# Performance work log

Hardware: AMD Instinct MI355X
Metric: run time of the kernel (lower is better)

The kernel has to match this reference:

```python
import jax, jax.numpy as jnp
import numpy as np

D_MODEL = 1024
MAX_ELEMENTS = 128


def setup_inputs() -> dict:
    key = jax.random.key(0)
    ks = jax.random.split(key, 12)
    B, S = 256, 128
    d, dq = D_MODEL, D_MODEL // 4
    inp = {
        "element_types": jax.random.randint(ks[0], (B, S), 0, 5, dtype=jnp.int64 if jax.config.jax_enable_x64 else jnp.int32),
        "element_indices": jax.random.randint(ks[1], (B, S), 0, MAX_ELEMENTS, dtype=jnp.int64 if jax.config.jax_enable_x64 else jnp.int32),
        "style_vectors": jax.random.normal(ks[2], (B, 5), dtype=jnp.float32),
        "page_captions": jax.random.normal(ks[3], (B, 768), dtype=jnp.float32),
        # learned parameters (torch Linear stored as [in, out] so y = x @ W + b)
        "type_emb": jax.random.normal(ks[4], (5, d), dtype=jnp.float32) * 0.02,
        "pos_emb": jax.random.normal(ks[5], (MAX_ELEMENTS, d), dtype=jnp.float32) * 0.02,
        "style_w1": jax.random.normal(ks[6], (5, dq), dtype=jnp.float32) * 0.02,
        "style_b1": jnp.zeros((dq,), dtype=jnp.float32),
        "style_w2": jax.random.normal(ks[7], (dq, d), dtype=jnp.float32) * 0.02,
        "style_b2": jnp.zeros((d,), dtype=jnp.float32),
        "text_w": jax.random.normal(ks[8], (768, d), dtype=jnp.float32) * 0.02,
        "text_b": jnp.zeros((d,), dtype=jnp.float32),
        "final_pos_emb": jax.random.normal(ks[9], (MAX_ELEMENTS, d), dtype=jnp.float32) * 0.02,
    }
    return inp


def reference(element_types, element_indices, style_vectors, page_captions,
              type_emb, pos_emb, style_w1, style_b1, style_w2, style_b2,
              text_w, text_b, final_pos_emb):
    B, S = element_types.shape
    # table gathers: [B, S, d]
    emb = type_emb[element_types] + pos_emb[element_indices]
    # per-batch style/text embeds computed ONCE (the torch loop recomputes them per step)
    style_embed = jnp.maximum(style_vectors @ style_w1 + style_b1, 0.0) @ style_w2 + style_b2  # [B, d]
    page_embed = page_captions @ text_w + text_b  # [B, d]
    # loop over i with mask (types[:, i] == 1) == broadcast masked add
    mask1 = (element_types == 1)[:, :, None]  # [B, S, 1]
    emb = emb + mask1 * (style_embed + page_embed)[:, None, :]
    # final positional encoding over positions 0..S-1
    emb = emb + final_pos_emb[:S][None, :, :]
    padding_mask = element_types == 0
    return emb, padding_mask
```

## Files before the change

kernel.cpp:

```cpp
#include <hip/hip_runtime.h>

#define D      1024
#define SEQ    128
#define BATCH  256
#define DQ     256
#define TEXTC  768

typedef float f32x4 __attribute__((ext_vector_type(4)));

__global__ __launch_bounds__(256) void gemm_fused(
    const float* __restrict__ style_vectors,
    const float* __restrict__ page_captions,
    const float* __restrict__ style_w1,
    const float* __restrict__ style_b1,
    const float* __restrict__ style_w2,
    const float* __restrict__ style_b2,
    const float* __restrict__ text_w,
    const float* __restrict__ text_b,
    float* __restrict__ part)
{
    __shared__ float As[16][68];
    __shared__ float Bs[16][68];

    const int m0  = blockIdx.x * 64;
    const int n0  = blockIdx.y * 64;
    const int z   = blockIdx.z;
    const int tid = threadIdx.x;
    const int tm  = tid >> 4;
    const int tn  = tid & 15;

    const int am = tid >> 2;
    const int ak = (tid & 3) * 4;

    float sv[5];
    if (z == 0) {
#pragma unroll
        for (int j = 0; j < 5; ++j) sv[j] = style_vectors[(m0 + am) * 5 + j];
    }

    float acc[4][4] = {};

    for (int kc = 0; kc < 256; kc += 16) {
        if (z == 0) {
            int k = kc + ak;
#pragma unroll
            for (int r = 0; r < 4; ++r) {
                float h = style_b1[k + r];
#pragma unroll
                for (int j = 0; j < 5; ++j)
                    h = fmaf(sv[j], style_w1[j * DQ + k + r], h);
                As[ak + r][am] = fmaxf(h, 0.0f);
            }
        } else {
            float4 av = *(const float4*)
                &page_captions[(m0 + am) * TEXTC + (z * 256 - DQ) + kc + ak];
            As[ak + 0][am] = av.x;
            As[ak + 1][am] = av.y;
            As[ak + 2][am] = av.z;
            As[ak + 3][am] = av.w;
        }
        {
            int kk   = tid >> 4;
            int nq   = (tid & 15) * 4;
            int krow = z * 256 + kc + kk;
            const float* Wrow = (z == 0) ? &style_w2[krow * D]
                                         : &text_w[(krow - DQ) * D];
            *(float4*)&Bs[kk][nq] = *(const float4*)&Wrow[n0 + nq];
        }
        __syncthreads();

#pragma unroll
        for (int kk = 0; kk < 16; ++kk) {
            f32x4 a4 = *(const f32x4*)&As[kk][tm * 4];
            f32x4 b4 = *(const f32x4*)&Bs[kk][tn * 4];
#pragma unroll
            for (int ii = 0; ii < 4; ++ii)
#pragma unroll
                for (int jj = 0; jj < 4; ++jj)
                    acc[ii][jj] = fmaf(a4[ii], b4[jj], acc[ii][jj]);
        }
        __syncthreads();
    }

    float* dst = part + (size_t)z * BATCH * D;
    const int n = n0 + tn * 4;
#pragma unroll
    for (int ii = 0; ii < 4; ++ii) {
        int m = m0 + tm * 4 + ii;
        f32x4 v = {acc[ii][0], acc[ii][1], acc[ii][2], acc[ii][3]};
        if (z == 0) {
            v[0] += style_b2[n + 0] + text_b[n + 0];
            v[1] += style_b2[n + 1] + text_b[n + 1];
            v[2] += style_b2[n + 2] + text_b[n + 2];
            v[3] += style_b2[n + 3] + text_b[n + 3];
        }
        *(f32x4*)&dst[m * D + n] = v;
    }
}

__global__ __launch_bounds__(256) void reduce_part(
    const float* __restrict__ part,
    float* __restrict__ comb)
{
    const int i = blockIdx.x * 256 + threadIdx.x;
    const f32x4* p = (const f32x4*)part;
    const int Q = BATCH * D / 4;
    f32x4 v = p[i] + p[i + Q] + p[i + 2 * Q] + p[i + 3 * Q];
    ((f32x4*)comb)[i] = v;
}

__global__ __launch_bounds__(256) void scatter_kernel(
    const int* __restrict__ types,
    const int* __restrict__ indices,
    const float* __restrict__ type_emb,
    const float* __restrict__ pos_emb,
    const float* __restrict__ final_pos_emb,
    const float* __restrict__ comb,
    float* __restrict__ out_emb,
    float* __restrict__ out_mask)
{
    const int bs = blockIdx.x;
    const int b  = bs >> 7;
    const int s  = bs & 127;
    const int et = types[bs];
    const int ei = indices[bs];
    const int tid = threadIdx.x;

    f32x4 t = ((const f32x4*)&type_emb[et * D])[tid];
    f32x4 p = ((const f32x4*)&pos_emb[ei * D])[tid];
    f32x4 f = ((const f32x4*)&final_pos_emb[s * D])[tid];
    f32x4 v = t + p + f;
    if (et == 1)
        v = v + ((const f32x4*)&comb[b * D])[tid];

    __builtin_nontemporal_store(v, &((f32x4*)out_emb)[bs * 256 + tid]);

    if (tid == 0)
        out_mask[bs] = (et == 0) ? 1.0f : 0.0f;
}

extern "C" void kernel_launch(void* const* d_in, const int* in_sizes, int n_in,
                              void* d_out, int out_size, void* d_ws, size_t ws_size,
                              hipStream_t stream) {
    const int*   element_types   = (const int*)  d_in[0];
    const int*   element_indices = (const int*)  d_in[1];
    const float* style_vectors   = (const float*)d_in[2];
    const float* page_captions   = (const float*)d_in[3];
    const float* type_emb        = (const float*)d_in[4];
    const float* pos_emb         = (const float*)d_in[5];
    const float* style_w1        = (const float*)d_in[6];
    const float* style_b1        = (const float*)d_in[7];
    const float* style_w2        = (const float*)d_in[8];
    const float* style_b2        = (const float*)d_in[9];
    const float* text_w          = (const float*)d_in[10];
    const float* text_b          = (const float*)d_in[11];
    const float* final_pos_emb   = (const float*)d_in[12];

    float* part = (float*)d_ws;
    float* comb = (float*)d_ws + 4 * BATCH * D;

    float* out_emb  = (float*)d_out;
    float* out_mask = (float*)d_out + BATCH * SEQ * D;

    gemm_fused<<<dim3(BATCH / 64, D / 64, 4), 256, 0, stream>>>(
        style_vectors, page_captions, style_w1, style_b1,
        style_w2, style_b2, text_w, text_b, part);

    reduce_part<<<BATCH * D / 4 / 256, 256, 0, stream>>>(part, comb);

    scatter_kernel<<<BATCH * SEQ, 256, 0, stream>>>(
        element_types, element_indices, type_emb, pos_emb, final_pos_emb,
        comb, out_emb, out_mask);
}
```

Measured before the change: 206.9 us.

## Halve GEMM M-tile, use nontemporal reduce loads, one wave per row in scatter

The GEMM tile shrinks from 64 to 32 rows, doubling the block count to 512 so more CUs have work; only half the threads now load the A tile. The reduce kernel reads its partials with nontemporal loads. The scatter kernel now assigns one wave per (b,s) row, four rows per block, so the grid is four times smaller and each lane handles four vectors. The style branch is hoisted so it is uniform per wave.

New measurement: 199.9 us, median of 2. 3.4% less time.

```diff
diff --git a/kernel.cpp b/kernel.cpp
--- a/kernel.cpp
+++ b/kernel.cpp
@@ -7,6 +7,7 @@
 #define TEXTC  768
 
 typedef float f32x4 __attribute__((ext_vector_type(4)));
+typedef float f32x2 __attribute__((ext_vector_type(2)));
 
 __global__ __launch_bounds__(256) void gemm_fused(
     const float* __restrict__ style_vectors,
@@ -19,10 +20,10 @@
     const float* __restrict__ text_b,
     float* __restrict__ part)
 {
-    __shared__ float As[16][68];
+    __shared__ float As[16][36];
     __shared__ float Bs[16][68];
 
-    const int m0  = blockIdx.x * 64;
+    const int m0  = blockIdx.x * 32;
     const int n0  = blockIdx.y * 64;
     const int z   = blockIdx.z;
     const int tid = threadIdx.x;
@@ -33,31 +34,33 @@
     const int ak = (tid & 3) * 4;
 
     float sv[5];
-    if (z == 0) {
+    if (z == 0 && tid < 128) {
 #pragma unroll
         for (int j = 0; j < 5; ++j) sv[j] = style_vectors[(m0 + am) * 5 + j];
     }
 
-    float acc[4][4] = {};
+    float acc[2][4] = {};
 
     for (int kc = 0; kc < 256; kc += 16) {
-        if (z == 0) {
-            int k = kc + ak;
+        if (tid < 128) {
+            if (z == 0) {
+                int k = kc + ak;
 #pragma unroll
-            for (int r = 0; r < 4; ++r) {
-                float h = style_b1[k + r];
+                for (int r = 0; r < 4; ++r) {
+                    float h = style_b1[k + r];
 #pragma unroll
-                for (int j = 0; j < 5; ++j)
-                    h = fmaf(sv[j], style_w1[j * DQ + k + r], h);
-                As[ak + r][am] = fmaxf(h, 0.0f);
+                    for (int j = 0; j < 5; ++j)
+                        h = fmaf(sv[j], style_w1[j * DQ + k + r], h);
+                    As[ak + r][am] = fmaxf(h, 0.0f);
+                }
+            } else {
+                float4 av = *(const float4*)
+                    &page_captions[(m0 + am) * TEXTC + (z * 256 - DQ) + kc + ak];
+                As[ak + 0][am] = av.x;
+                As[ak + 1][am] = av.y;
+                As[ak + 2][am] = av.z;
+                As[ak + 3][am] = av.w;
             }
-        } else {
-            float4 av = *(const float4*)
-                &page_captions[(m0 + am) * TEXTC + (z * 256 - DQ) + kc + ak];
-            As[ak + 0][am] = av.x;
-            As[ak + 1][am] = av.y;
-            As[ak + 2][am] = av.z;
-            As[ak + 3][am] = av.w;
         }
         {
             int kk   = tid >> 4;
@@ -71,13 +74,13 @@
 
 #pragma unroll
         for (int kk = 0; kk < 16; ++kk) {
-            f32x4 a4 = *(const f32x4*)&As[kk][tm * 4];
+            f32x2 a2 = *(const f32x2*)&As[kk][tm * 2];
             f32x4 b4 = *(const f32x4*)&Bs[kk][tn * 4];
 #pragma unroll
-            for (int ii = 0; ii < 4; ++ii)
+            for (int ii = 0; ii < 2; ++ii)
 #pragma unroll
                 for (int jj = 0; jj < 4; ++jj)
-                    acc[ii][jj] = fmaf(a4[ii], b4[jj], acc[ii][jj]);
+                    acc[ii][jj] = fmaf(a2[ii], b4[jj], acc[ii][jj]);
         }
         __syncthreads();
     }
@@ -85,8 +88,8 @@
     float* dst = part + (size_t)z * BATCH * D;
     const int n = n0 + tn * 4;
 #pragma unroll
-    for (int ii = 0; ii < 4; ++ii) {
-        int m = m0 + tm * 4 + ii;
+    for (int ii = 0; ii < 2; ++ii) {
+        int m = m0 + tm * 2 + ii;
         f32x4 v = {acc[ii][0], acc[ii][1], acc[ii][2], acc[ii][3]};
         if (z == 0) {
             v[0] += style_b2[n + 0] + text_b[n + 0];
@@ -105,7 +108,10 @@
     const int i = blockIdx.x * 256 + threadIdx.x;
     const f32x4* p = (const f32x4*)part;
     const int Q = BATCH * D / 4;
-    f32x4 v = p[i] + p[i + Q] + p[i + 2 * Q] + p[i + 3 * Q];
+    f32x4 v = __builtin_nontemporal_load(&p[i])
+            + __builtin_nontemporal_load(&p[i + Q])
+            + __builtin_nontemporal_load(&p[i + 2 * Q])
+            + __builtin_nontemporal_load(&p[i + 3 * Q]);
     ((f32x4*)comb)[i] = v;
 }
 
@@ -119,23 +125,38 @@
     float* __restrict__ out_emb,
     float* __restrict__ out_mask)
 {
-    const int bs = blockIdx.x;
-    const int b  = bs >> 7;
-    const int s  = bs & 127;
-    const int et = types[bs];
-    const int ei = indices[bs];
-    const int tid = threadIdx.x;
+    const int tid  = threadIdx.x;
+    const int wave = tid >> 6;
+    const int lane = tid & 63;
+    const int bs   = blockIdx.x * 4 + wave;
+    const int b    = bs >> 7;
+    const int s    = bs & 127;
+    const int et   = types[bs];
+    const int ei   = indices[bs];
 
-    f32x4 t = ((const f32x4*)&type_emb[et * D])[tid];
-    f32x4 p = ((const f32x4*)&pos_emb[ei * D])[tid];
-    f32x4 f = ((const f32x4*)&final_pos_emb[s * D])[tid];
-    f32x4 v = t + p + f;
-    if (et == 1)
-        v = v + ((const f32x4*)&comb[b * D])[tid];
+    const f32x4* te = (const f32x4*)&type_emb[et * D];
+    const f32x4* pe = (const f32x4*)&pos_emb[ei * D];
+    const f32x4* fe = (const f32x4*)&final_pos_emb[s * D];
+    f32x4* dst = (f32x4*)out_emb + (size_t)bs * 256;
 
-    __builtin_nontemporal_store(v, &((f32x4*)out_emb)[bs * 256 + tid]);
+    if (et == 1) {
+        const f32x4* cb = (const f32x4*)&comb[b * D];
+#pragma unroll
+        for (int j = 0; j < 4; ++j) {
+            int idx = lane + 64 * j;
+            f32x4 v = te[idx] + pe[idx] + fe[idx] + cb[idx];
+            __builtin_nontemporal_store(v, &dst[idx]);
+        }
+    } else {
+#pragma unroll
+        for (int j = 0; j < 4; ++j) {
+            int idx = lane + 64 * j;
+            f32x4 v = te[idx] + pe[idx] + fe[idx];
+            __builtin_nontemporal_store(v, &dst[idx]);
+        }
+    }
 
-    if (tid == 0)
+    if (lane == 0)
         out_mask[bs] = (et == 0) ? 1.0f : 0.0f;
 }
 
@@ -162,13 +183,13 @@
     float* out_emb  = (float*)d_out;
     float* out_mask = (float*)d_out + BATCH * SEQ * D;
 
-    gemm_fused<<<dim3(BATCH / 64, D / 64, 4), 256, 0, stream>>>(
+    gemm_fused<<<dim3(BATCH / 32, D / 64, 4), 256, 0, stream>>>(
         style_vectors, page_captions, style_w1, style_b1,
         style_w2, style_b2, text_w, text_b, part);
 
     reduce_part<<<BATCH * D / 4 / 256, 256, 0, stream>>>(part, comb);
 
-    scatter_kernel<<<BATCH * SEQ, 256, 0, stream>>>(
+    scatter_kernel<<<BATCH * SEQ / 4, 256, 0, stream>>>(
         element_types, element_indices, type_emb, pos_emb, final_pos_emb,
         comb, out_emb, out_mask);
 }
```
